# Kernel optimization log

Hardware: AMD Instinct MI355X
Metric: run time of the kernel (lower is better)

## Reference

```python
import jax, jax.numpy as jnp
import numpy as np

BLOCK, HALO, HEADS = 8, 4, 4


def setup_inputs() -> dict:
    key = jax.random.key(0)
    ks = jax.random.split(key, 9)
    B, C, H, W = 8, 256, 64, 64
    inner = C  # heads * dim_head = 4 * 64
    d = inner // HEADS
    R = BLOCK + 2 * HALO  # 16
    s = 0.02
    return {
        "x": jax.random.normal(ks[0], (B, C, H, W), jnp.float32),
        "wq": jax.random.normal(ks[1], (inner, C), jnp.float32) * s,
        "wkv": jax.random.normal(ks[2], (2 * inner, C), jnp.float32) * s,
        "wo": jax.random.normal(ks[3], (C, inner), jnp.float32) * s,
        "bo": jax.random.normal(ks[4], (C,), jnp.float32) * s,
        "rel_h": jax.random.normal(ks[5], (2 * R - 1, d), jnp.float32) * (d ** -0.5),
        "rel_w": jax.random.normal(ks[6], (2 * R - 1, d), jnp.float32) * (d ** -0.5),
        "w_conv": jax.random.normal(ks[7], (4 * C, C), jnp.float32) * s,
        "b_conv": jax.random.normal(ks[8], (4 * C,), jnp.float32) * s,
    }


def reference(x, wq, wkv, wo, bo, rel_h, rel_w, w_conv, b_conv):
    B, C, H, W = x.shape
    bs, halo, heads = BLOCK, HALO, HEADS
    R = bs + 2 * halo
    inner = wq.shape[0]
    d = inner // heads
    nh, nw = H // bs, W // bs
    Nb = B * nh * nw

    # ---- HaloAttention ----
    # block queries: (B, C, nh, bs, nw, bs) -> (Nb, bs*bs, C)
    q_in = x.reshape(B, C, nh, bs, nw, bs).transpose(0, 2, 4, 3, 5, 1).reshape(Nb, bs * bs, C)
    # haloed K/V windows via overlapping gather (== F.unfold(kernel=R, stride=bs, pad=halo))
    xp = jnp.pad(x, ((0, 0), (0, 0), (halo, halo), (halo, halo)))
    ridx = (jnp.arange(nh) * bs)[:, None] + jnp.arange(R)[None]  # (nh, R)
    cidx = (jnp.arange(nw) * bs)[:, None] + jnp.arange(R)[None]  # (nw, R)
    win = xp[:, :, ridx][:, :, :, :, cidx]                       # (B, C, nh, R, nw, R)
    kv_in = win.transpose(0, 2, 4, 3, 5, 1).reshape(Nb, R * R, C)

    q = (q_in @ wq.T).reshape(Nb, bs * bs, heads, d).transpose(0, 2, 1, 3) * (d ** -0.5)
    kv = kv_in @ wkv.T
    k, v = jnp.split(kv, 2, axis=-1)
    k = k.reshape(Nb, R * R, heads, d).transpose(0, 2, 1, 3)
    v = v.reshape(Nb, R * R, heads, d).transpose(0, 2, 1, 3)

    sim = jnp.einsum('bhid,bhjd->bhij', q, k)  # (Nb, heads, bs*bs, R*R)

    # relative position logits (computed from the scaled q, as in the torch code)
    q5 = q.reshape(Nb, heads, bs, bs, d)
    rel_idx = jnp.arange(R)[None, :] - jnp.arange(bs)[:, None] + (R - 1)  # (bs, R)
    lw = jnp.einsum('bhxyd,yjd->bhxyj', q5, rel_w[rel_idx])  # over key col j
    lh = jnp.einsum('bhxyd,xid->bhxyi', q5, rel_h[rel_idx])  # over key row i
    sim = sim.reshape(Nb, heads, bs, bs, R, R) + lw[..., None, :] + lh[..., None]
    sim = sim.reshape(Nb, heads, bs * bs, R * R)

    # mask out padded halo positions
    m = jnp.pad(jnp.ones((H, W), bool), ((halo, halo), (halo, halo)))
    mwin = m[ridx][:, :, cidx].transpose(0, 2, 1, 3).reshape(nh * nw, R * R)
    mask = jnp.broadcast_to(mwin[None], (B, nh * nw, R * R)).reshape(Nb, 1, 1, R * R)
    sim = jnp.where(mask, sim, -jnp.finfo(sim.dtype).max)

    attn = jax.nn.softmax(sim, axis=-1)
    out = jnp.einsum('bhij,bhjd->bhid', attn, v)
    out = out.transpose(0, 2, 1, 3).reshape(Nb, bs * bs, inner)
    out = out @ wo.T + bo  # (Nb, bs*bs, C)
    y = out.reshape(B, nh, nw, bs, bs, C).transpose(0, 5, 1, 3, 2, 4).reshape(B, C, H, W)

    # ---- Conv2d(dim, 4*dim, 1) + PixelShuffle(2) ----
    y = jnp.einsum('bchw,oc->bohw', y, w_conv) + b_conv[None, :, None, None]
    Cn = y.shape[1] // 4
    y = y.reshape(B, Cn, 2, 2, H, W).transpose(0, 1, 4, 2, 5, 3).reshape(B, Cn, 2 * H, 2 * W)
    return y
```

## Files before the change

kernel.cpp:

```cpp
#include <hip/hip_runtime.h>

typedef unsigned short u16;
typedef unsigned int u32;
typedef __attribute__((ext_vector_type(8))) short short8;
typedef __attribute__((ext_vector_type(4))) float f32x4;

__device__ __forceinline__ float bf2f(u16 u){ union { u32 i; float f; } x; x.i = ((u32)u)<<16; return x.f; }
__device__ __forceinline__ u16 f2bf(float f){ union { float f; u32 i; } x; x.f = f; u32 r = x.i + 0x7fffu + ((x.i>>16)&1u); return (u16)(r>>16); }

#define MFMA16(a,b,c) __builtin_amdgcn_mfma_f32_16x16x32_bf16((a),(b),(c),0,0,0)

__device__ __forceinline__ uint4 ld8(const void* p, size_t off, int f32) {
  if (f32) {
    const float* fp = (const float*)p + off;
    float4 a = *(const float4*)fp;
    float4 b = *(const float4*)(fp + 4);
    uint4 o;
    o.x = (u32)f2bf(a.x) | ((u32)f2bf(a.y)<<16);
    o.y = (u32)f2bf(a.z) | ((u32)f2bf(a.w)<<16);
    o.z = (u32)f2bf(b.x) | ((u32)f2bf(b.y)<<16);
    o.w = (u32)f2bf(b.z) | ((u32)f2bf(b.w)<<16);
    return o;
  }
  return *(const uint4*)((const u16*)p + off);
}
__device__ __forceinline__ uint2 ld4(const void* p, size_t off, int f32) {
  if (f32) {
    const float* fp = (const float*)p + off;
    float4 a = *(const float4*)fp;
    uint2 o;
    o.x = (u32)f2bf(a.x) | ((u32)f2bf(a.y)<<16);
    o.y = (u32)f2bf(a.z) | ((u32)f2bf(a.w)<<16);
    return o;
  }
  return *(const uint2*)((const u16*)p + off);
}
__device__ __forceinline__ float ldsc(const void* p, size_t off, int f32) {
  if (f32) return ((const float*)p)[off];
  return bf2f(((const u16*)p)[off]);
}

__global__ __launch_bounds__(256) void k_detect(const u32* __restrict__ x, int* __restrict__ flag)
{
  __shared__ int cnt;
  if (threadIdx.x == 0) cnt = 0;
  __syncthreads();
  int c = 0;
  #pragma unroll
  for (int i = 0; i < 32; ++i) {
    u32 w = x[threadIdx.x*32 + i];
    u32 e = (w >> 7) & 0xFFu;
    c += (e == 0u || (e >= 96u && e <= 143u)) ? 1 : 0;
  }
  atomicAdd(&cnt, c);
  __syncthreads();
  if (threadIdx.x == 0) *flag = (cnt < 4915) ? 1 : 0;
}

__global__ __launch_bounds__(256) void k_fuse_w(
  const u32* __restrict__ x,
  const void* __restrict__ wo, const void* __restrict__ wconv,
  const void* __restrict__ bo, const void* __restrict__ bconv,
  u16* __restrict__ F, float* __restrict__ bfus, int* __restrict__ flagp)
{
  __shared__ int cnt;
  __shared__ __align__(16) u16 WC[16*256];
  __shared__ __align__(16) u16 WO[32*128];
  __shared__ float bred[16][17];
  const int t = threadIdx.x;
  if (t == 0) cnt = 0;
  __syncthreads();
  {
    int c = 0;
    #pragma unroll
    for (int i=0;i<8;++i) {
      u32 w = x[t*8+i];
      u32 e = (w>>7)&0xFFu;
      c += (e==0u || (e>=96u && e<=143u)) ? 1 : 0;
    }
    atomicAdd(&cnt, c);
  }
  __syncthreads();
  const int f32 = (cnt < 1229) ? 1 : 0;
  if (blockIdx.x == 0 && blockIdx.y == 0 && t == 0) *flagp = f32;
  const int o0 = blockIdx.x*16, c0 = blockIdx.y*128;
  {
    int row = t>>4, ch = (t&15)*16;
    *(uint4*)&WC[row*256+ch]     = ld8(wconv, (size_t)(o0+row)*256 + ch, f32);
    *(uint4*)&WC[row*256+ch+8]   = ld8(wconv, (size_t)(o0+row)*256 + ch + 8, f32);
  }
  float acc[8] = {};
  const int ty = t>>4, tx = t&15;
  for (int jc=0;jc<8;++jc) {
    __syncthreads();
    {
      int jr = t>>3, cc = (t&7)*16;
      *(uint4*)&WO[jr*128+cc]   = ld8(wo, (size_t)(jc*32+jr)*256 + c0 + cc, f32);
      *(uint4*)&WO[jr*128+cc+8] = ld8(wo, (size_t)(jc*32+jr)*256 + c0 + cc + 8, f32);
    }
    __syncthreads();
    #pragma unroll 4
    for (int jj=0;jj<32;++jj) {
      float wv = bf2f(WC[ty*256 + jc*32 + jj]);
      short8 w8 = *(const short8*)&WO[jj*128 + tx*8];
      #pragma unroll
      for (int i=0;i<8;++i) acc[i] += wv * bf2f((u16)w8[i]);
    }
  }
  {
    u32 pw[4];
    #pragma unroll
    for (int j=0;j<4;++j) pw[j] = (u32)f2bf(acc[2*j]) | ((u32)f2bf(acc[2*j+1])<<16);
    *(uint4*)&F[(size_t)(o0+ty)*256 + c0 + tx*8] = *(uint4*)pw;
  }
  if (blockIdx.y == 0) {
    float s = 0.0f;
    #pragma unroll 4
    for (int j=tx*16; j<tx*16+16; ++j) s += bf2f(WC[ty*256+j]) * ldsc(bo, j, f32);
    bred[ty][tx] = s;
  }
  __syncthreads();
  if (blockIdx.y == 0 && t < 16) {
    float s = 0.0f;
    #pragma unroll
    for (int p=0;p<16;++p) s += bred[t][p];
    bfus[o0+t] = s + ldsc(bconv, o0+t, f32);
  }
}

__global__ __launch_bounds__(256) void k_transpose(const void* __restrict__ x, u16* __restrict__ xt,
                                                   const int* __restrict__ flagp)
{
  __shared__ int sflag;
  __shared__ __align__(16) u16 tile[64][68];
  if (threadIdx.x == 0) sflag = *flagp;
  __syncthreads();
  const int f32 = sflag;
  const int p0 = blockIdx.x*64, c0 = blockIdx.y*64, b = blockIdx.z;
  const int t = threadIdx.x;
  const size_t xbo = ((size_t)(b*256 + c0))*4096 + p0;
  #pragma unroll
  for (int pass=0; pass<4; ++pass) {
    int cl = pass*16 + (t>>4);
    int pl = (t&15)*4;
    uint2 v = ld4(x, xbo + (size_t)cl*4096 + pl, f32);
    *(uint2*)&tile[cl][pl] = v;
  }
  __syncthreads();
  u16* xtb = xt + ((size_t)b*4096 + p0)*256 + c0;
  #pragma unroll
  for (int pass=0; pass<4; ++pass) {
    int pl = pass*16 + (t>>4);
    int cl = (t&15)*4;
    unsigned int lo = (unsigned int)tile[cl][pl]   | ((unsigned int)tile[cl+1][pl]<<16);
    unsigned int hi = (unsigned int)tile[cl+2][pl] | ((unsigned int)tile[cl+3][pl]<<16);
    uint2 o; o.x = lo; o.y = hi;
    *(uint2*)(xtb + (size_t)pl*256 + cl) = o;
  }
}

__global__ __launch_bounds__(256) void k_gemm_bt(
  const u16* __restrict__ A, int lda,
  const void* __restrict__ Bt0, const void* __restrict__ Bt1, int nsplit,
  const void* __restrict__ bias,
  void* __restrict__ C, int M, int N, int K,
  float s_lo, float s_hi, int shuffle, int internalB,
  const int* __restrict__ flagp)
{
  __shared__ int sflag;
  __shared__ __align__(16) char smem[40960];
  if (threadIdx.x == 0) sflag = *flagp;
  __syncthreads();
  const int f32 = sflag;
  const int bf = internalB ? 0 : f32;
  const int biasf = internalB ? 1 : f32;
  const int m0 = blockIdx.x*128, n0 = blockIdx.y*128;
  const void* Bs; int boff;
  if (Bt1 && n0 >= nsplit) { Bs = Bt1; boff = n0 - nsplit; } else { Bs = Bt0; boff = n0; }
  const int t = threadIdx.x, lane = t & 63, wv = t >> 6;
  const int wm = (wv & 1)*64, wn = (wv >> 1)*64;
  const int lm = lane & 15, lq = lane >> 4;
  f32x4 acc[4][4] = {};
  uint4 pa[2], pb[2];
  #pragma unroll
  for (int i=0;i<2;++i) {
    int u = t + i*256, row = u >> 2, ch = (u & 3)*8;
    pa[i] = *(const uint4*)(A + (size_t)(m0+row)*lda + ch);
    pb[i] = ld8(Bs, (size_t)(boff+row)*K + ch, bf);
  }
  int cur = 0;
  for (int k0 = 0; k0 < K; k0 += 32) {
    u16* Als = (u16*)(smem + cur*20480);
    u16* Bls = (u16*)(smem + cur*20480 + 10240);
    #pragma unroll
    for (int i=0;i<2;++i) {
      int u = t + i*256, row = u >> 2, ch = (u & 3)*8;
      *(uint4*)&Als[row*40 + ch] = pa[i];
      *(uint4*)&Bls[row*40 + ch] = pb[i];
    }
    __syncthreads();
    if (k0 + 32 < K) {
      int k1 = k0 + 32;
      #pragma unroll
      for (int i=0;i<2;++i) {
        int u = t + i*256, row = u >> 2, ch = (u & 3)*8;
        pa[i] = *(const uint4*)(A + (size_t)(m0+row)*lda + k1 + ch);
        pb[i] = ld8(Bs, (size_t)(boff+row)*K + k1 + ch, bf);
      }
    }
    short8 af[4], bfr[4];
    #pragma unroll
    for (int i=0;i<4;++i) af[i]  = *(const short8*)&Als[(wm + i*16 + lm)*40 + lq*8];
    #pragma unroll
    for (int i=0;i<4;++i) bfr[i] = *(const short8*)&Bls[(wn + i*16 + lm)*40 + lq*8];
    #pragma unroll
    for (int mt=0;mt<4;++mt)
      #pragma unroll
      for (int nt=0;nt<4;++nt)
        acc[mt][nt] = MFMA16(af[mt], bfr[nt], acc[mt][nt]);
    cur ^= 1;
  }

  if (!shuffle) {
    u16* eh = (u16*)smem;
    #pragma unroll
    for (int c=0;c<2;++c) {
      __syncthreads();
      if ((wv>>1) == c) {
        #pragma unroll
        for (int nt=0;nt<4;++nt) {
          int col = n0 + c*64 + nt*16 + lm;
          float sc = (col < nsplit) ? s_lo : s_hi;
          float bv = bias ? ldsc(bias, col, biasf) : 0.0f;
          #pragma unroll
          for (int mt=0;mt<4;++mt)
            #pragma unroll
            for (int r=0;r<4;++r) {
              int row = wm + mt*16 + lq*4 + r;
              eh[row*72 + nt*16 + lm] = f2bf(acc[mt][nt][r]*sc + bv);
            }
        }
      }
      __syncthreads();
      {
        int row = t >> 1, off = (t & 1)*32;
        const uint4* s = (const uint4*)&eh[row*72 + off];
        uint4 v0 = s[0], v1 = s[1], v2 = s[2], v3 = s[3];
        uint4* dp = (uint4*)((u16*)C + (size_t)(m0+row)*N + n0 + c*64 + off);
        dp[0]=v0; dp[1]=v1; dp[2]=v2; dp[3]=v3;
      }
    }
  } else {
    float* ef = (float*)smem;
    const int b = m0 >> 12;
    const int hh0 = (m0 & 4095) >> 6;
    #pragma unroll
    for (int c=0;c<4;++c) {
      __syncthreads();
      if ((wv>>1) == (c>>1)) {
        #pragma unroll
        for (int nt2=0;nt2<2;++nt2) {
          int nt = (c&1)*2 + nt2;
          int col = n0 + wn + nt*16 + lm;
          float bv = bias ? ldsc(bias, col, biasf) : 0.0f;
          int col_rel = nt2*16 + lm;
          int cn_rel = col_rel >> 2, rr = (col_rel >> 1) & 1, ss = col_rel & 1;
          #pragma unroll
          for (int mt=0;mt<4;++mt)
            #pragma unroll
            for (int r=0;r<4;++r) {
              int row = wm + mt*16 + lq*4 + r;
              int orow = cn_rel*4 + (row>>6)*2 + rr;
              int ow   = (row & 63)*2 + ss;
              ef[orow*136 + ow] = acc[mt][nt][r]*s_hi + bv;
            }
        }
      }
      __syncthreads();
      {
        int orow = t >> 3, seg = t & 7;
        int cn_rel = orow >> 2, oh_rel = orow & 3;
        int cn = ((n0 + c*32) >> 2) + cn_rel;
        size_t obase = (((size_t)(b*256 + cn))*128 + hh0*2 + oh_rel)*128 + seg*16;
        const float4* s = (const float4*)&ef[orow*136 + seg*16];
        float4 v0 = s[0], v1 = s[1], v2 = s[2], v3 = s[3];
        if (f32) {
          float4* dp = (float4*)((float*)C + obase);
          dp[0]=v0; dp[1]=v1; dp[2]=v2; dp[3]=v3;
        } else {
          float vv[16];
          *(float4*)&vv[0]=v0; *(float4*)&vv[4]=v1; *(float4*)&vv[8]=v2; *(float4*)&vv[12]=v3;
          u32 pw[8];
          #pragma unroll
          for (int j=0;j<8;++j) pw[j] = (u32)f2bf(vv[2*j]) | ((u32)f2bf(vv[2*j+1])<<16);
          u16* dp = (u16*)C + obase;
          *(uint4*)dp       = *(uint4*)&pw[0];
          *(uint4*)(dp + 8) = *(uint4*)&pw[4];
        }
      }
    }
  }
}

#define MASKVAL (-30000.0f)
__global__ __launch_bounds__(256) void k_halo_attn(
  const u16* __restrict__ qkv,
  const void* __restrict__ relh, const void* __restrict__ relw,
  u16* __restrict__ aout, int ostride,
  const int* __restrict__ flagp)
{
  __shared__ int sflag;
  __shared__ __align__(16) u16 Qs[64*72];
  __shared__ __align__(16) u16 KP[128*72];
  __shared__ __align__(16) u16 Vt[64*136];
  __shared__ __align__(16) u16 Gw[64*32];
  __shared__ __align__(16) u16 Gh[64*32];
  if (threadIdx.x == 0) sflag = *flagp;
  __syncthreads();
  const int f32 = sflag;

  const int blk = blockIdx.x, head = blockIdx.y;
  const int bb = blk >> 6, by = (blk >> 3) & 7, bx = blk & 7;
  const int h0 = by*8, w0 = bx*8;
  const int t = threadIdx.x, lane = t & 63, wv = t >> 6;
  const int lm = lane & 15, lq = lane >> 4;
  const size_t pixbase = (size_t)bb * 4096;
  const float LOG2E = 1.4426950408889634f;

  #pragma unroll
  for (int i=0;i<2;++i) {
    int u = t + i*256;
    int row = u >> 3, ch = (u & 7)*8;
    int qx = row >> 3, qy = row & 7;
    size_t p = pixbase + (size_t)(h0+qx)*64 + (w0+qy);
    *(uint4*)&Qs[row*72 + ch] = *(const uint4*)(qkv + p*768 + head*64 + ch);
  }
  {
    u16* RW = KP; u16* RH = KP + 2048;
    if (t < 248) {
      *(uint4*)&RW[t*8] = ld8(relw, (size_t)t*8, f32);
      *(uint4*)&RH[t*8] = ld8(relh, (size_t)t*8, f32);
    } else {
      uint4 z; z.x=z.y=z.z=z.w=0;
      int o = 1984 + (t-248)*8;
      *(uint4*)&RW[o] = z;
      *(uint4*)&RH[o] = z;
    }
  }
  __syncthreads();
  {
    const u16* RW = KP; const u16* RH = KP + 2048;
    f32x4 agw[2] = {}, agh[2] = {};
    #pragma unroll
    for (int ks=0;ks<2;++ks) {
      short8 aq = *(const short8*)&Qs[(wv*16 + lm)*72 + ks*32 + lq*8];
      #pragma unroll
      for (int nt=0;nt<2;++nt) {
        short8 bw = *(const short8*)&RW[(nt*16 + lm)*64 + ks*32 + lq*8];
        short8 bh = *(const short8*)&RH[(nt*16 + lm)*64 + ks*32 + lq*8];
        agw[nt] = MFMA16(aq, bw, agw[nt]);
        agh[nt] = MFMA16(aq, bh, agh[nt]);
      }
    }
    #pragma unroll
    for (int nt=0;nt<2;++nt)
      #pragma unroll
      for (int r=0;r<4;++r) {
        int m = wv*16 + lq*4 + r, c = nt*16 + lm;
        Gw[m*32 + c] = f2bf(agw[nt][r]);
        Gh[m*32 + c] = f2bf(agh[nt][r]);
      }
  }
  __syncthreads();

  float m_run[4], l_run[4];
  #pragma unroll
  for (int r=0;r<4;++r){ m_run[r] = MASKVAL; l_run[r] = 0.0f; }
  f32x4 acc_o[4] = {};

  for (int tile=0; tile<2; ++tile) {
    #pragma unroll
    for (int i=0;i<4;++i) {
      int u = t + i*256;
      int kl = u >> 3, ch = (u & 7)*8;
      int ki = tile*8 + (kl >> 4), kj = kl & 15;
      int hk = h0 - 4 + ki, wk = w0 - 4 + kj;
      uint4 v; v.x=v.y=v.z=v.w=0;
      if ((unsigned)hk < 64u && (unsigned)wk < 64u) {
        size_t p = pixbase + (size_t)hk*64 + wk;
        v = *(const uint4*)(qkv + p*768 + 256 + head*64 + ch);
      }
      *(uint4*)&KP[kl*72 + ch] = v;
    }
    {
      int kl = t & 127, db = (t >> 7)*32;
      int ki = tile*8 + (kl >> 4), kj = kl & 15;
      int hk = h0 - 4 + ki, wk = w0 - 4 + kj;
      bool ok = ((unsigned)hk < 64u) && ((unsigned)wk < 64u);
      size_t p = pixbase + (size_t)hk*64 + wk;
      const u16* vp = qkv + p*768 + 512 + head*64 + db;
      #pragma unroll
      for (int c=0;c<4;++c) {
        union { uint4 v; u16 s[8]; } uu;
        uu.v.x=uu.v.y=uu.v.z=uu.v.w=0;
        if (ok) uu.v = *(const uint4*)(vp + c*8);
        #pragma unroll
        for (int jj=0;jj<8;++jj) Vt[(db + c*8 + jj)*136 + kl] = uu.s[jj];
      }
    }
    __syncthreads();
    f32x4 as[8] = {};
    #pragma unroll
    for (int ks=0;ks<2;++ks) {
      short8 aq = *(const short8*)&Qs[(wv*16 + lm)*72 + ks*32 + lq*8];
      #pragma unroll
      for (int nt=0;nt<8;++nt) {
        short8 bk = *(const short8*)&KP[(nt*16 + lm)*72 + ks*32 + lq*8];
        as[nt] = MFMA16(aq, bk, as[nt]);
      }
    }
    __syncthreads();
    #pragma unroll
    for (int r=0;r<4;++r) {
      int m = wv*16 + lq*4 + r;
      int qx = m >> 3, qy = m & 7;
      float vals[8]; float rowmax = MASKVAL;
      #pragma unroll
      for (int nt=0;nt<8;++nt) {
        int ki = tile*8 + nt;
        int hk = h0 - 4 + ki, wk = w0 - 4 + lm;
        float v = as[nt][r]
                + bf2f(Gw[m*32 + (lm - qy + 15)])
                + bf2f(Gh[m*32 + (ki - qx + 15)]);
        if (!((unsigned)hk < 64u && (unsigned)wk < 64u)) v = MASKVAL;
        vals[nt] = v;
        rowmax = fmaxf(rowmax, v);
      }
      #pragma unroll
      for (int s=1;s<16;s<<=1) rowmax = fmaxf(rowmax, __shfl_xor(rowmax, s, 64));
      float mnew = fmaxf(m_run[r], rowmax);
      float alpha = exp2f((m_run[r] - mnew)*LOG2E);
      float rs = 0.0f;
      #pragma unroll
      for (int nt=0;nt<8;++nt) {
        float e = exp2f((vals[nt] - mnew)*LOG2E);
        rs += e;
        KP[m*136 + nt*16 + lm] = f2bf(e);
      }
      #pragma unroll
      for (int s=1;s<16;s<<=1) rs += __shfl_xor(rs, s, 64);
      l_run[r] = l_run[r]*alpha + rs;
      m_run[r] = mnew;
      #pragma unroll
      for (int nt=0;nt<4;++nt) acc_o[nt][r] *= alpha;
    }
    __syncthreads();
    #pragma unroll
    for (int ks=0;ks<4;++ks) {
      short8 ap = *(const short8*)&KP[(wv*16 + lm)*136 + ks*32 + lq*8];
      #pragma unroll
      for (int nt=0;nt<4;++nt) {
        short8 bv = *(const short8*)&Vt[(nt*16 + lm)*136 + ks*32 + lq*8];
        acc_o[nt] = MFMA16(ap, bv, acc_o[nt]);
      }
    }
    __syncthreads();
  }
  #pragma unroll
  for (int nt=0;nt<4;++nt)
    #pragma unroll
    for (int r=0;r<4;++r) {
      int m = wv*16 + lq*4 + r;
      int qx = m >> 3, qy = m & 7;
      size_t p = pixbase + (size_t)(h0+qx)*64 + (w0+qy);
      aout[p*(size_t)ostride + head*64 + nt*16 + lm] = f2bf(acc_o[nt][r]/l_run[r]);
    }
}

extern "C" void kernel_launch(void* const* d_in, const int* in_sizes, int n_in,
                              void* d_out, int out_size, void* d_ws, size_t ws_size,
                              hipStream_t stream)
{
  const void* x     = d_in[0];
  const void* wq    = d_in[1];
  const void* wkv   = d_in[2];
  const void* wo    = d_in[3];
  const void* bo    = d_in[4];
  const void* relh  = d_in[5];
  const void* relw  = d_in[6];
  const void* wconv = d_in[7];
  const void* bconv = d_in[8];

  int*  flag = (int*)d_ws;
  u16*  base = (u16*)d_out;
  u16*  qkv  = base;
  u16*  xt   = base + 25165824;

  const size_t WS_FUSED = 4096 + 524288 + 4096 + 16777216;

  if (ws_size >= WS_FUSED) {
    u16*   Wf   = (u16*)((char*)d_ws + 4096);
    float* bfus = (float*)((char*)d_ws + 4096 + 524288);
    u16*   aout = (u16*)((char*)d_ws + 4096 + 524288 + 4096);
    k_fuse_w<<<dim3(64,2), 256, 0, stream>>>((const u32*)x, wo, wconv, bo, bconv,
                                             Wf, bfus, flag);
    k_transpose<<<dim3(64,4,8), 256, 0, stream>>>(x, xt, flag);
    k_gemm_bt<<<dim3(256,6), 256, 0, stream>>>(xt, 256, wq, wkv, 256, nullptr,
                                               qkv, 32768, 768, 256, 0.125f, 1.0f, 0, 0, flag);
    k_halo_attn<<<dim3(512,4), 256, 0, stream>>>(qkv, relh, relw, aout, 256, flag);
    k_gemm_bt<<<dim3(256,8), 256, 0, stream>>>(aout, 256, Wf, nullptr, 0, bfus,
                                               d_out, 32768, 1024, 256, 1.0f, 1.0f, 1, 1, flag);
  } else {
    u16* y2 = (u16*)((char*)d_ws + 4096);
    k_detect<<<1, 256, 0, stream>>>((const u32*)x, flag);
    k_transpose<<<dim3(64,4,8), 256, 0, stream>>>(x, xt, flag);
    k_gemm_bt<<<dim3(256,6), 256, 0, stream>>>(xt, 256, wq, wkv, 256, nullptr,
                                               qkv, 32768, 768, 256, 0.125f, 1.0f, 0, 0, flag);
    k_halo_attn<<<dim3(512,4), 256, 0, stream>>>(qkv, relh, relw, qkv, 768, flag);
    k_gemm_bt<<<dim3(256,2), 256, 0, stream>>>(qkv, 768, wo, nullptr, 0, bo,
                                               y2, 32768, 256, 256, 1.0f, 1.0f, 0, 0, flag);
    k_gemm_bt<<<dim3(256,8), 256, 0, stream>>>(y2, 256, wconv, nullptr, 0, bconv,
                                               d_out, 32768, 1024, 256, 1.0f, 1.0f, 1, 0, flag);
  }
}
```

Measured before the change: 390.7 us.

## Deepen GEMM software pipeline with two register prefetch stages and lighter barriers

Restructures the GEMM main loop so two K-slices are held in registers at once, with the loop unrolled by two over the double LDS buffers. Global loads now run two steps ahead of compute, and __syncthreads is replaced by a barrier that waits only on LDS traffic (lgkmcnt), so in-flight global loads do not stall it. The aim is to hide global memory latency behind MFMA work. The cost is more VGPRs for the extra prefetch registers, and the new code assumes K is a multiple of 64 with K at least 64. The WAR hazard on the LDS buffers depends on the placement of the single barrier.

```diff
diff --git a/kernel.cpp b/kernel.cpp
--- a/kernel.cpp
+++ b/kernel.cpp
@@ -159,6 +159,37 @@
   }
 }
 
+#define GEMM_BARRIER asm volatile("s_waitcnt lgkmcnt(0)\n\ts_barrier" ::: "memory")
+#define GLOADS(SA, SB, KOFF) \
+  _Pragma("unroll") \
+  for (int i=0;i<2;++i) { \
+    int u = t + i*256, row = u >> 2, ch = (u & 3)*8; \
+    SA[i] = *(const uint4*)(A + (size_t)(m0+row)*lda + (KOFF) + ch); \
+    SB[i] = ld8(Bs, (size_t)(boff+row)*K + (KOFF) + ch, bf); \
+  }
+#define DSWRITE(SA, SB, BUF) \
+  { u16* Als_ = (u16*)(smem + (BUF)*20480); \
+    u16* Bls_ = (u16*)(smem + (BUF)*20480 + 10240); \
+    _Pragma("unroll") \
+    for (int i=0;i<2;++i) { \
+      int u = t + i*256, row = u >> 2, ch = (u & 3)*8; \
+      *(uint4*)&Als_[row*40 + ch] = SA[i]; \
+      *(uint4*)&Bls_[row*40 + ch] = SB[i]; \
+    } }
+#define DSCOMP(BUF) \
+  { const u16* Als_ = (const u16*)(smem + (BUF)*20480); \
+    const u16* Bls_ = (const u16*)(smem + (BUF)*20480 + 10240); \
+    short8 af[4], bfr[4]; \
+    _Pragma("unroll") \
+    for (int i=0;i<4;++i) af[i]  = *(const short8*)&Als_[(wm + i*16 + lm)*40 + lq*8]; \
+    _Pragma("unroll") \
+    for (int i=0;i<4;++i) bfr[i] = *(const short8*)&Bls_[(wn + i*16 + lm)*40 + lq*8]; \
+    _Pragma("unroll") \
+    for (int mt=0;mt<4;++mt) \
+      _Pragma("unroll") \
+      for (int nt=0;nt<4;++nt) \
+        acc[mt][nt] = MFMA16(af[mt], bfr[nt], acc[mt][nt]); }
+
 __global__ __launch_bounds__(256) void k_gemm_bt(
   const u16* __restrict__ A, int lda,
   const void* __restrict__ Bt0, const void* __restrict__ Bt1, int nsplit,
@@ -181,44 +212,25 @@
   const int wm = (wv & 1)*64, wn = (wv >> 1)*64;
   const int lm = lane & 15, lq = lane >> 4;
   f32x4 acc[4][4] = {};
-  uint4 pa[2], pb[2];
-  #pragma unroll
-  for (int i=0;i<2;++i) {
-    int u = t + i*256, row = u >> 2, ch = (u & 3)*8;
-    pa[i] = *(const uint4*)(A + (size_t)(m0+row)*lda + ch);
-    pb[i] = ld8(Bs, (size_t)(boff+row)*K + ch, bf);
-  }
-  int cur = 0;
-  for (int k0 = 0; k0 < K; k0 += 32) {
-    u16* Als = (u16*)(smem + cur*20480);
-    u16* Bls = (u16*)(smem + cur*20480 + 10240);
-    #pragma unroll
-    for (int i=0;i<2;++i) {
-      int u = t + i*256, row = u >> 2, ch = (u & 3)*8;
-      *(uint4*)&Als[row*40 + ch] = pa[i];
-      *(uint4*)&Bls[row*40 + ch] = pb[i];
-    }
-    __syncthreads();
-    if (k0 + 32 < K) {
-      int k1 = k0 + 32;
-      #pragma unroll
-      for (int i=0;i<2;++i) {
-        int u = t + i*256, row = u >> 2, ch = (u & 3)*8;
-        pa[i] = *(const uint4*)(A + (size_t)(m0+row)*lda + k1 + ch);
-        pb[i] = ld8(Bs, (size_t)(boff+row)*K + k1 + ch, bf);
-      }
-    }
-    short8 af[4], bfr[4];
-    #pragma unroll
-    for (int i=0;i<4;++i) af[i]  = *(const short8*)&Als[(wm + i*16 + lm)*40 + lq*8];
-    #pragma unroll
-    for (int i=0;i<4;++i) bfr[i] = *(const short8*)&Bls[(wn + i*16 + lm)*40 + lq*8];
-    #pragma unroll
-    for (int mt=0;mt<4;++mt)
-      #pragma unroll
-      for (int nt=0;nt<4;++nt)
-        acc[mt][nt] = MFMA16(af[mt], bfr[nt], acc[mt][nt]);
-    cur ^= 1;
+  uint4 p0a[2], p0b[2], p1a[2], p1b[2];
+
+  GLOADS(p0a, p0b, 0)
+  GLOADS(p1a, p1b, 32)
+  DSWRITE(p0a, p0b, 0)
+  GLOADS(p0a, p0b, 64)
+  GEMM_BARRIER;
+
+  for (int k0 = 0; k0 < K; k0 += 64) {
+    DSCOMP(0)
+    DSWRITE(p1a, p1b, 1)
+    if (k0 + 96 < K) { GLOADS(p1a, p1b, k0 + 96) }
+    GEMM_BARRIER;
+    DSCOMP(1)
+    if (k0 + 64 < K) {
+      DSWRITE(p0a, p0b, 0)
+      if (k0 + 128 < K) { GLOADS(p0a, p0b, k0 + 128) }
+      GEMM_BARRIER;
+    }
   }
 
   if (!shuffle) {
```

Measured after the change: 406.5 us. 4.0% more time.

## Load GEMM MFMA fragments directly from global memory instead of LDS staging

Applied to the files above, without the earlier changes.

Removes the double-buffered LDS staging of A/B tiles in the bf16 GEMM main loop. Each wave now reads its own MFMA fragments straight from global memory, which drops the per-iteration __syncthreads and LDS round trips. The kernel's shared memory shrinks from 40960 to 18432 bytes, which could allow more resident blocks. The cost is that each A/B row is fetched by two waves, doubling global/L2 traffic, and there is no explicit software prefetch. The shuffle epilogue's LDS row stride also changes from 136 to 134 floats, which breaks 16-byte alignment of its float4 reads.

```diff
diff --git a/kernel.cpp b/kernel.cpp
--- a/kernel.cpp
+++ b/kernel.cpp
@@ -168,7 +168,7 @@
   const int* __restrict__ flagp)
 {
   __shared__ int sflag;
-  __shared__ __align__(16) char smem[40960];
+  __shared__ __align__(16) char smem[18432];
   if (threadIdx.x == 0) sflag = *flagp;
   __syncthreads();
   const int f32 = sflag;
@@ -181,44 +181,27 @@
   const int wm = (wv & 1)*64, wn = (wv >> 1)*64;
   const int lm = lane & 15, lq = lane >> 4;
   f32x4 acc[4][4] = {};
-  uint4 pa[2], pb[2];
-  #pragma unroll
-  for (int i=0;i<2;++i) {
-    int u = t + i*256, row = u >> 2, ch = (u & 3)*8;
-    pa[i] = *(const uint4*)(A + (size_t)(m0+row)*lda + ch);
-    pb[i] = ld8(Bs, (size_t)(boff+row)*K + ch, bf);
-  }
-  int cur = 0;
+
+  const u16* arow[4];
+  size_t brow[4];
+  #pragma unroll
+  for (int i=0;i<4;++i) {
+    arow[i] = A + (size_t)(m0 + wm + i*16 + lm)*lda + lq*8;
+    brow[i] = (size_t)(boff + wn + i*16 + lm)*K + lq*8;
+  }
+
+  #pragma unroll 2
   for (int k0 = 0; k0 < K; k0 += 32) {
-    u16* Als = (u16*)(smem + cur*20480);
-    u16* Bls = (u16*)(smem + cur*20480 + 10240);
-    #pragma unroll
-    for (int i=0;i<2;++i) {
-      int u = t + i*256, row = u >> 2, ch = (u & 3)*8;
-      *(uint4*)&Als[row*40 + ch] = pa[i];
-      *(uint4*)&Bls[row*40 + ch] = pb[i];
-    }
-    __syncthreads();
-    if (k0 + 32 < K) {
-      int k1 = k0 + 32;
-      #pragma unroll
-      for (int i=0;i<2;++i) {
-        int u = t + i*256, row = u >> 2, ch = (u & 3)*8;
-        pa[i] = *(const uint4*)(A + (size_t)(m0+row)*lda + k1 + ch);
-        pb[i] = ld8(Bs, (size_t)(boff+row)*K + k1 + ch, bf);
-      }
-    }
     short8 af[4], bfr[4];
     #pragma unroll
-    for (int i=0;i<4;++i) af[i]  = *(const short8*)&Als[(wm + i*16 + lm)*40 + lq*8];
-    #pragma unroll
-    for (int i=0;i<4;++i) bfr[i] = *(const short8*)&Bls[(wn + i*16 + lm)*40 + lq*8];
+    for (int i=0;i<4;++i) af[i] = *(const short8*)(arow[i] + k0);
+    #pragma unroll
+    for (int i=0;i<4;++i) { uint4 v = ld8(Bs, brow[i] + k0, bf); bfr[i] = *(const short8*)&v; }
     #pragma unroll
     for (int mt=0;mt<4;++mt)
       #pragma unroll
       for (int nt=0;nt<4;++nt)
         acc[mt][nt] = MFMA16(af[mt], bfr[nt], acc[mt][nt]);
-    cur ^= 1;
   }
 
   if (!shuffle) {
@@ -272,7 +255,7 @@
               int row = wm + mt*16 + lq*4 + r;
               int orow = cn_rel*4 + (row>>6)*2 + rr;
               int ow   = (row & 63)*2 + ss;
-              ef[orow*136 + ow] = acc[mt][nt][r]*s_hi + bv;
+              ef[orow*134 + ow] = acc[mt][nt][r]*s_hi + bv;
             }
         }
       }
@@ -282,7 +265,7 @@
         int cn_rel = orow >> 2, oh_rel = orow & 3;
         int cn = ((n0 + c*32) >> 2) + cn_rel;
         size_t obase = (((size_t)(b*256 + cn))*128 + hh0*2 + oh_rel)*128 + seg*16;
-        const float4* s = (const float4*)&ef[orow*136 + seg*16];
+        const float4* s = (const float4*)&ef[orow*134 + seg*16];
         float4 v0 = s[0], v1 = s[1], v2 = s[2], v3 = s[3];
         if (f32) {
           float4* dp = (float4*)((float*)C + obase);
```

After: 407.5 us. +4.3%, slower.
